# Optimization experiments

Hardware: AMD Instinct MI355X
Metric: run time of the kernel (lower is better)

Reference implementation:

```python
import jax, jax.numpy as jnp
import numpy as np

IN_FEATURES = 4096
OUT_FEATURES = 4096
R = 16

def setup_inputs() -> dict:
    key = jax.random.key(0)
    k1, k2 = jax.random.split(key)
    x = jax.random.normal(k1, (4, 2048, IN_FEATURES), dtype=jnp.float32)
    # Original init: B = zeros, A = randn. Use randn for B too so the output
    # is non-trivial for correctness testing (math is identical regardless).
    lora_matrix_B = jax.random.normal(k2, (OUT_FEATURES, R), dtype=jnp.float32) * 0.02
    lora_matrix_A = jax.random.normal(jax.random.fold_in(key, 1), (R, IN_FEATURES), dtype=jnp.float32)
    return {"x": x, "lora_matrix_B": lora_matrix_B, "lora_matrix_A": lora_matrix_A}

def reference(x, lora_matrix_B, lora_matrix_A):
    # lora_weights = B @ A  -> [out_features, in_features]
    lora_weights = jnp.matmul(lora_matrix_B, lora_matrix_A)
    # F.linear(x, W) = x @ W^T
    return jnp.einsum('bsi,oi->bso', x, lora_weights)
```

## Files before the change

kernel.cpp:

```cpp
#include <hip/hip_runtime.h>

#define K_DIM   4096
#define N_DIM   4096
#define M_ROWS  8192
#define KF      (K_DIM / 4)
#define NF      (N_DIM / 4)
#define KSPLIT  4
#define TPART_F4_STRIDE (M_ROWS * 16 / 4)

__global__ __launch_bounds__(256) void transpose_B(const float* __restrict__ B,
                                                   float* __restrict__ Bt) {
    const int i = blockIdx.x * 256 + threadIdx.x;
    const int r = i >> 12;
    const int c = i & (N_DIM - 1);
    Bt[i] = B[c * 16 + r];
}

__global__ __launch_bounds__(256, 4) void lora_xat(const float* __restrict__ x,
                                                   const float* __restrict__ A,
                                                   float* __restrict__ tpart) {
    const int tid  = threadIdx.x;
    const int wv   = tid >> 6;
    const int lane = tid & 63;
    const int rb   = blockIdx.x >> 2;
    const int h    = blockIdx.x & 3;
    const int row0 = rb * 16 + wv * 4;
    const int kbase = h * 256;

    const float4* x4 = (const float4*)x;
    const float4* A4 = (const float4*)A;

    float red[64];
    #pragma unroll
    for (int v = 0; v < 64; ++v) red[v] = 0.f;

    for (int it = 0; it < 4; ++it) {
        const int kf = kbase + it * 64 + lane;
        float4 xv[4];
        #pragma unroll
        for (int j = 0; j < 4; ++j)
            xv[j] = x4[(size_t)(row0 + j) * KF + kf];
        #pragma unroll
        for (int r = 0; r < 16; ++r) {
            const float4 av = A4[r * KF + kf];
            #pragma unroll
            for (int j = 0; j < 4; ++j) {
                float a = red[j * 16 + r];
                a = fmaf(xv[j].x, av.x, a);
                a = fmaf(xv[j].y, av.y, a);
                a = fmaf(xv[j].z, av.z, a);
                a = fmaf(xv[j].w, av.w, a);
                red[j * 16 + r] = a;
            }
        }
    }

    #pragma unroll
    for (int s = 0; s < 6; ++s) {
        const int m = 1 << s;
        const int b = (lane >> s) & 1;
        #pragma unroll
        for (int u = 0; u < (64 >> (s + 1)); ++u) {
            const float lo = red[2 * u];
            const float hi = red[2 * u + 1];
            const float send = b ? lo : hi;
            const float recv = __shfl_xor(send, m, 64);
            const float kept = b ? hi : lo;
            red[u] = kept + recv;
        }
    }

    tpart[((size_t)h * M_ROWS + row0) * 16 + lane] = red[0];
}

__global__ __launch_bounds__(256, 4) void lora_tb(const float* __restrict__ tpart,
                                                  const float* __restrict__ Bt,
                                                  float* __restrict__ out) {
    const int tid = threadIdx.x;
    const int rb  = blockIdx.x >> 2;
    const int cb  = blockIdx.x & 3;

    __shared__ float4 t_s4[64];
    if (tid < 64) {
        const float4* p4 = (const float4*)tpart;
        float4 s = p4[(size_t)rb * 64 + tid];
        #pragma unroll
        for (int hh = 1; hh < KSPLIT; ++hh) {
            const float4 q = p4[(size_t)hh * TPART_F4_STRIDE + rb * 64 + tid];
            s.x += q.x; s.y += q.y; s.z += q.z; s.w += q.w;
        }
        t_s4[tid] = s;
    }

    const int c4 = cb * 256 + tid;
    const float4* Bt4 = (const float4*)Bt;
    float4 bv[16];
    #pragma unroll
    for (int r = 0; r < 16; ++r)
        bv[r] = Bt4[r * NF + c4];

    __syncthreads();

    float4* out4 = (float4*)out;
    const float* t_s = (const float*)t_s4;

    #pragma unroll
    for (int row = 0; row < 16; ++row) {
        float4 tq[4];
        #pragma unroll
        for (int q = 0; q < 4; ++q)
            tq[q] = t_s4[row * 4 + q];
        float4 o = {0.f, 0.f, 0.f, 0.f};
        #pragma unroll
        for (int r = 0; r < 16; ++r) {
            const float4 tv4 = tq[r >> 2];
            const float tv = ((r & 3) == 0) ? tv4.x :
                             ((r & 3) == 1) ? tv4.y :
                             ((r & 3) == 2) ? tv4.z : tv4.w;
            o.x = fmaf(tv, bv[r].x, o.x);
            o.y = fmaf(tv, bv[r].y, o.y);
            o.z = fmaf(tv, bv[r].z, o.z);
            o.w = fmaf(tv, bv[r].w, o.w);
        }
        out4[(size_t)(rb * 16 + row) * NF + c4] = o;
    }
    (void)t_s;
}

extern "C" void kernel_launch(void* const* d_in, const int* in_sizes, int n_in,
                              void* d_out, int out_size, void* d_ws, size_t ws_size,
                              hipStream_t stream) {
    const float* x = (const float*)d_in[0];
    const float* B = (const float*)d_in[1];
    const float* A = (const float*)d_in[2];
    float* out = (float*)d_out;

    float* Bt    = (float*)d_ws;
    float* tpart = Bt + 16 * N_DIM;

    transpose_B<<<(N_DIM * 16) / 256, 256, 0, stream>>>(B, Bt);
    lora_xat<<<(M_ROWS / 16) * KSPLIT, 256, 0, stream>>>(x, A, tpart);
    lora_tb<<<(M_ROWS / 16) * (N_DIM / 1024), 256, 0, stream>>>(tpart, Bt, out);
}
```

Baseline: 77.29 us.

## Stage A slices in LDS, double K-split, and drop the B transpose kernel

The x·A^T kernel now splits K eight ways and stages each block's A slice in shared memory, so A is no longer re-read from global memory per wavefront. The B transpose launch is removed: the output kernel loads B rows directly into registers, with each thread computing four consecutive output columns. Partial sums from the eight K-splits are reduced in two stages through shared memory. The aim is to cut one kernel launch and redundant global traffic, at the cost of more partial-sum traffic and extra LDS use per block.

```diff
diff --git a/kernel.cpp b/kernel.cpp
--- a/kernel.cpp
+++ b/kernel.cpp
@@ -5,44 +5,52 @@
 #define M_ROWS  8192
 #define KF      (K_DIM / 4)
 #define NF      (N_DIM / 4)
-#define KSPLIT  4
-#define TPART_F4_STRIDE (M_ROWS * 16 / 4)
-
-__global__ __launch_bounds__(256) void transpose_B(const float* __restrict__ B,
-                                                   float* __restrict__ Bt) {
-    const int i = blockIdx.x * 256 + threadIdx.x;
-    const int r = i >> 12;
-    const int c = i & (N_DIM - 1);
-    Bt[i] = B[c * 16 + r];
-}
+#define KSPLIT  8
+#define KCH     (KF / KSPLIT)
+#define NTILES  (M_ROWS / 16)
+#define TP_F4_STRIDE (M_ROWS * 16 / 4)
 
 __global__ __launch_bounds__(256, 4) void lora_xat(const float* __restrict__ x,
                                                    const float* __restrict__ A,
                                                    float* __restrict__ tpart) {
+    __shared__ float4 Alds[16 * KCH];
+
     const int tid  = threadIdx.x;
     const int wv   = tid >> 6;
     const int lane = tid & 63;
-    const int rb   = blockIdx.x >> 2;
-    const int h    = blockIdx.x & 3;
+    const int rb   = blockIdx.x >> 3;
+    const int h    = blockIdx.x & 7;
     const int row0 = rb * 16 + wv * 4;
-    const int kbase = h * 256;
+    const int kbase = h * KCH;
 
     const float4* x4 = (const float4*)x;
     const float4* A4 = (const float4*)A;
+
+    #pragma unroll
+    for (int i = 0; i < 8; ++i) {
+        const int idx = i * 256 + tid;
+        const int r = idx >> 7;
+        const int c = idx & (KCH - 1);
+        Alds[idx] = A4[r * KF + kbase + c];
+    }
 
     float red[64];
     #pragma unroll
     for (int v = 0; v < 64; ++v) red[v] = 0.f;
 
-    for (int it = 0; it < 4; ++it) {
-        const int kf = kbase + it * 64 + lane;
+    __syncthreads();
+
+    #pragma unroll
+    for (int it = 0; it < 2; ++it) {
+        const int kl = it * 64 + lane;
+        const int kf = kbase + kl;
         float4 xv[4];
         #pragma unroll
         for (int j = 0; j < 4; ++j)
             xv[j] = x4[(size_t)(row0 + j) * KF + kf];
         #pragma unroll
         for (int r = 0; r < 16; ++r) {
-            const float4 av = A4[r * KF + kf];
+            const float4 av = Alds[r * KCH + kl];
             #pragma unroll
             for (int j = 0; j < 4; ++j) {
                 float a = red[j * 16 + r];
@@ -74,35 +82,47 @@
 }
 
 __global__ __launch_bounds__(256, 4) void lora_tb(const float* __restrict__ tpart,
-                                                  const float* __restrict__ Bt,
+                                                  const float* __restrict__ B,
                                                   float* __restrict__ out) {
+    __shared__ float4 tp_s[4][64];
+    __shared__ float4 t_s4[64];
+
     const int tid = threadIdx.x;
     const int rb  = blockIdx.x >> 2;
     const int cb  = blockIdx.x & 3;
 
-    __shared__ float4 t_s4[64];
+    const int o0 = cb * 1024 + tid * 4;
+    float4 breg[4][4];
+    const float4* B4 = (const float4*)B;
+    #pragma unroll
+    for (int j = 0; j < 4; ++j)
+        #pragma unroll
+        for (int q = 0; q < 4; ++q)
+            breg[j][q] = B4[(size_t)(o0 + j) * 4 + q];
+
+    {
+        const int f  = tid & 63;
+        const int hp = tid >> 6;
+        const float4* p4 = (const float4*)tpart;
+        float4 a = p4[(size_t)(2 * hp) * TP_F4_STRIDE + rb * 64 + f];
+        const float4 b = p4[(size_t)(2 * hp + 1) * TP_F4_STRIDE + rb * 64 + f];
+        a.x += b.x; a.y += b.y; a.z += b.z; a.w += b.w;
+        tp_s[hp][f] = a;
+    }
+    __syncthreads();
     if (tid < 64) {
-        const float4* p4 = (const float4*)tpart;
-        float4 s = p4[(size_t)rb * 64 + tid];
+        float4 s = tp_s[0][tid];
         #pragma unroll
-        for (int hh = 1; hh < KSPLIT; ++hh) {
-            const float4 q = p4[(size_t)hh * TPART_F4_STRIDE + rb * 64 + tid];
+        for (int hp = 1; hp < 4; ++hp) {
+            const float4 q = tp_s[hp][tid];
             s.x += q.x; s.y += q.y; s.z += q.z; s.w += q.w;
         }
         t_s4[tid] = s;
     }
-
-    const int c4 = cb * 256 + tid;
-    const float4* Bt4 = (const float4*)Bt;
-    float4 bv[16];
-    #pragma unroll
-    for (int r = 0; r < 16; ++r)
-        bv[r] = Bt4[r * NF + c4];
-
     __syncthreads();
 
     float4* out4 = (float4*)out;
-    const float* t_s = (const float*)t_s4;
+    const int c4 = cb * 256 + tid;
 
     #pragma unroll
     for (int row = 0; row < 16; ++row) {
@@ -110,21 +130,21 @@
         #pragma unroll
         for (int q = 0; q < 4; ++q)
             tq[q] = t_s4[row * 4 + q];
-        float4 o = {0.f, 0.f, 0.f, 0.f};
+        float o0v = 0.f, o1v = 0.f, o2v = 0.f, o3v = 0.f;
         #pragma unroll
         for (int r = 0; r < 16; ++r) {
             const float4 tv4 = tq[r >> 2];
             const float tv = ((r & 3) == 0) ? tv4.x :
                              ((r & 3) == 1) ? tv4.y :
                              ((r & 3) == 2) ? tv4.z : tv4.w;
-            o.x = fmaf(tv, bv[r].x, o.x);
-            o.y = fmaf(tv, bv[r].y, o.y);
-            o.z = fmaf(tv, bv[r].z, o.z);
-            o.w = fmaf(tv, bv[r].w, o.w);
+            o0v = fmaf(tv, ((const float*)&breg[0][0])[r], o0v);
+            o1v = fmaf(tv, ((const float*)&breg[1][0])[r], o1v);
+            o2v = fmaf(tv, ((const float*)&breg[2][0])[r], o2v);
+            o3v = fmaf(tv, ((const float*)&breg[3][0])[r], o3v);
         }
+        const float4 o = {o0v, o1v, o2v, o3v};
         out4[(size_t)(rb * 16 + row) * NF + c4] = o;
     }
-    (void)t_s;
 }
 
 extern "C" void kernel_launch(void* const* d_in, const int* in_sizes, int n_in,
@@ -135,10 +155,8 @@
     const float* A = (const float*)d_in[2];
     float* out = (float*)d_out;
 
-    float* Bt    = (float*)d_ws;
-    float* tpart = Bt + 16 * N_DIM;
+    float* tpart = (float*)d_ws;
 
-    transpose_B<<<(N_DIM * 16) / 256, 256, 0, stream>>>(B, Bt);
-    lora_xat<<<(M_ROWS / 16) * KSPLIT, 256, 0, stream>>>(x, A, tpart);
-    lora_tb<<<(M_ROWS / 16) * (N_DIM / 1024), 256, 0, stream>>>(tpart, Bt, out);
+    lora_xat<<<NTILES * KSPLIT, 256, 0, stream>>>(x, A, tpart);
+    lora_tb<<<NTILES * (N_DIM / 1024), 256, 0, stream>>>(tpart, B, out);
 }
```

Measured after the change: 66.07 us. 14.5% less time.
